# Kernel tuning notes

Hardware: AMD Instinct MI355X
Metric: run time of the kernel (lower is better)

## Reference

```python
import jax, jax.numpy as jnp
import numpy as np

N, M, H, EMB, F = 2000, 32, 64, 32, 32   # nodes, neighbors, hidden, emb_dim, node_feat_dim
T, B, HOR = 12, 4, 12                     # seq_len, batch, horizon
K = 2                                     # tcn kernel
L_SAGE = 2
DILS = (1, 2)                             # dilations for the 2 TCN blocks


def _causal_conv(x, w, b, d):
    # x: (BN, C, T), w: (C_out, C_in, K) -- causal via left padding (K-1)*d
    y = jax.lax.conv_general_dilated(
        x, w, window_strides=(1,), padding=[((K - 1) * d, 0)],
        rhs_dilation=(d,), dimension_numbers=('NCH', 'OIH', 'NCH'))
    return y + b[None, :, None]


def setup_inputs() -> dict:
    key = jax.random.key(0)
    ks = jax.random.split(key, 32)
    s = 0.05
    def g(i, shape):
        return jax.random.normal(ks[i], shape, dtype=jnp.float32) * s
    return dict(
        inputs=jax.random.normal(ks[0], (T, B, N), dtype=jnp.float32),
        node_feas=jax.random.normal(ks[1], (N, F), dtype=jnp.float32),
        node_index=jax.random.randint(ks[2], (N, M), 0, N),
        # NodeEmbeddingMLP (fc3/fc4/fc5)
        w_fc3=g(3, (F, H)), b_fc3=jnp.zeros((H,), jnp.float32),
        w_fc4=g(4, (H, H)), b_fc4=jnp.zeros((H,), jnp.float32),
        w_fc5=g(5, (H, EMB)), b_fc5=jnp.zeros((EMB,), jnp.float32),
        # node_hidden_proj
        w_nhp=g(6, (EMB, H)), b_nhp=jnp.zeros((H,), jnp.float32),
        # attention (no bias)
        w_q=g(7, (EMB, H)), w_k=g(8, (EMB, H)),
        # input_proj
        w_in=g(9, (1, H)), b_in=jnp.zeros((H,), jnp.float32),
        # GraphSAGE layers (stacked)
        sage_w_self=g(10, (L_SAGE, H, H)), sage_b_self=jnp.zeros((L_SAGE, H), jnp.float32),
        sage_w_neigh=g(11, (L_SAGE, H, H)), sage_b_neigh=jnp.zeros((L_SAGE, H), jnp.float32),
        # TCN: 2 temporal blocks, each with conv1/conv2 (OIH layout)
        tcn_w1=g(12, (2, H, H, K)), tcn_b1=jnp.zeros((2, H), jnp.float32),
        tcn_w2=g(13, (2, H, H, K)), tcn_b2=jnp.zeros((2, H), jnp.float32),
        # scalar gate + output head
        w_gate=g(14, (H, 1)), b_gate=jnp.zeros((1,), jnp.float32),
        w_out=g(15, (H, HOR)), b_out=jnp.zeros((HOR,), jnp.float32),
    )


def reference(inputs, node_feas, node_index,
              w_fc3, b_fc3, w_fc4, b_fc4, w_fc5, b_fc5,
              w_nhp, b_nhp, w_q, w_k, w_in, b_in,
              sage_w_self, sage_b_self, sage_w_neigh, sage_b_neigh,
              tcn_w1, tcn_b1, tcn_w2, tcn_b2,
              w_gate, b_gate, w_out, b_out):
    # --- node embedding MLP ---
    e = jax.nn.relu(node_feas @ w_fc3 + b_fc3)
    e = jax.nn.relu(e @ w_fc4 + b_fc4)
    e = e @ w_fc5 + b_fc5                                  # (N, EMB)

    # --- attention over sampled neighbors (learned slim adjacency) ---
    q = e @ w_q                                            # (N, H)
    k = e[node_index] @ w_k                                # (N, M, H)
    scores = jnp.einsum('nh,nmh->nm', q, k) / jnp.sqrt(jnp.float32(H))
    w_adj = jax.nn.softmax(scores, axis=1)                 # (N, M) rows sum to 1

    node_hidden = e @ w_nhp + b_nhp                        # (N, H)

    # --- reshape inputs: (T, B, N) -> (B, T, N, 1) ---
    x = jnp.transpose(inputs, (1, 0, 2)).reshape(B, T, N, 1)
    x_proj = x @ w_in + b_in                               # (B, T, N, H)
    fused = x_proj + node_hidden                           # broadcast (N, H)
    h = fused.reshape(B * T, N, H)

    # --- GraphSAGE encoder: gather neighbors, weighted aggregate ---
    for l in range(L_SAGE):
        nb = h[:, node_index]                              # (B*T, N, M, H) irregular gather
        agg = jnp.einsum('nm,bnmh->bnh', w_adj, nb)        # (B*T, N, H)
        h = jax.nn.relu(h @ sage_w_self[l] + sage_b_self[l]
                        + agg @ sage_w_neigh[l] + sage_b_neigh[l])

    mid_output = h.reshape(B, T, N, H)

    # --- TCN over time per node: (B*N, H, T) ---
    ht = jnp.transpose(mid_output, (0, 2, 3, 1)).reshape(B * N, H, T)
    for l in range(2):
        res = ht
        y = jax.nn.relu(_causal_conv(ht, tcn_w1[l], tcn_b1[l], DILS[l]))
        y = jax.nn.relu(_causal_conv(y, tcn_w2[l], tcn_b2[l], DILS[l]))
        ht = jax.nn.relu(y + res)

    h_t = ht[:, :, -1]                                     # (B*N, H) last step temporal
    h_s = mid_output[:, -1].reshape(B * N, H)              # (B*N, H) last step spatial
    gate = jax.nn.sigmoid(h_t @ w_gate + b_gate)           # (B*N, 1) scalar gate
    fused_out = gate * h_t + (1.0 - gate) * h_s

    out = fused_out @ w_out + b_out                        # (B*N, HOR)
    outputs = out.reshape(B, N, HOR).transpose(2, 0, 1).reshape(HOR, B, N)
    return outputs, mid_output, w_adj
```

## Files before the change

kernel.cpp:

```cpp
#include <hip/hip_runtime.h>
#include <math.h>


__global__ __launch_bounds__(256) void k_embed(
    const float* __restrict__ nf, const float* __restrict__ inputs,
    const float* __restrict__ w3, const float* __restrict__ b3,
    const float* __restrict__ w4, const float* __restrict__ b4,
    const float* __restrict__ w5, const float* __restrict__ b5,
    const float* __restrict__ wq, const float* __restrict__ wk,
    const float* __restrict__ wn, const float* __restrict__ bn,
    const float* __restrict__ b_in,
    const float* __restrict__ tw1, const float* __restrict__ tw2,
    const float* __restrict__ sws, const float* __restrict__ swn,
    float2* __restrict__ wtx, float4* __restrict__ wsg,
    float* __restrict__ qo, float* __restrict__ eko, float* __restrict__ nho,
    float* __restrict__ xT)
{
    const int tid = threadIdx.x;
    if (tid < 192) {
        const int id = blockIdx.x * 192 + tid;
        const int t = id / 8000, rem = id % 8000;
        const int b = rem / 2000, n2 = rem % 2000;
        xT[n2 * 48 + b * 12 + t] = inputs[id];
    }
    if (blockIdx.x < 64) {
        const int id = blockIdx.x * 256 + tid;
        const int c = id >> 12, rr = id & 4095;
        const int i = rr >> 6, o = rr & 63;
        const float* src = (c == 0) ? tw1 : (c == 1) ? tw2
                         : (c == 2) ? tw1 + 8192 : tw2 + 8192;
        wtx[id] = make_float2(src[o * 128 + i * 2], src[o * 128 + i * 2 + 1]);
    } else if (blockIdx.x < 80) {
        const int id = (blockIdx.x - 64) * 256 + tid;
        const int l = id >> 11, rr = id & 2047;
        const int k2 = rr >> 6, h = rr & 63;
        const float* S = sws + l * 4096;
        const float* Nn = swn + l * 4096;
        wsg[id] = make_float4(S[(2 * k2) * 64 + h],     Nn[(2 * k2) * 64 + h],
                              S[(2 * k2 + 1) * 64 + h], Nn[(2 * k2 + 1) * 64 + h]);
    }
    const int lane = tid & 63;
    const int n = blockIdx.x * 4 + (tid >> 6);

    float nfv = 0.f;
    if (lane < 32) nfv = nf[n * 32 + lane];

    float e1 = b3[lane];
#pragma unroll
    for (int f = 0; f < 32; ++f)
        e1 = fmaf(__shfl(nfv, f), w3[f * 64 + lane], e1);
    e1 = fmaxf(e1, 0.f);

    float e2 = b4[lane];
#pragma unroll
    for (int f = 0; f < 64; ++f)
        e2 = fmaf(__shfl(e1, f), w4[f * 64 + lane], e2);
    e2 = fmaxf(e2, 0.f);

    const int c = lane & 31;
    float ev = b5[c];
#pragma unroll
    for (int f = 0; f < 64; ++f)
        ev = fmaf(__shfl(e2, f), w5[f * 32 + c], ev);

    float qv = 0.f, ekv = 0.f, nhv = bn[lane] + b_in[lane];
#pragma unroll
    for (int f = 0; f < 32; ++f) {
        float e = __shfl(ev, f);
        qv  = fmaf(e, wq[f * 64 + lane], qv);
        ekv = fmaf(e, wk[f * 64 + lane], ekv);
        nhv = fmaf(e, wn[f * 64 + lane], nhv);
    }
    qo [n * 64 + lane] = qv;
    eko[n * 64 + lane] = ekv;
    nho[n * 64 + lane] = nhv;
}

__global__ __launch_bounds__(256) void k_front(
    const float* __restrict__ q, const float* __restrict__ ek,
    const float* __restrict__ xT, const float* __restrict__ nh2,
    const int* __restrict__ nidx,
    const float* __restrict__ sws, const float* __restrict__ sbs,
    const float* __restrict__ swn, const float* __restrict__ sbn,
    const float* __restrict__ w_in, const float4* __restrict__ wsg,
    float* __restrict__ wadj, float2* __restrict__ xa,
    float* __restrict__ base1, float* __restrict__ vecs)
{
    const int tid = threadIdx.x;
    const int lane = tid & 63, wave = tid >> 6;
    if (blockIdx.x == 500) {
        if (wave == 0) {
            const float wv = w_in[lane];
            float s1 = 0.f, n1 = 0.f;
#pragma unroll
            for (int k = 0; k < 64; ++k) {
                const float wkk = __shfl(wv, k);
                s1 = fmaf(wkk, sws[k * 64 + lane], s1);
                n1 = fmaf(wkk, swn[k * 64 + lane], n1);
            }
            vecs[lane] = s1; vecs[64 + lane] = n1;
        }
        return;
    }
    __shared__ __align__(16) float2 pair[4][64];
    const int n = blockIdx.x * 4 + wave;

    int j = 0;
    if (lane < 32) j = nidx[n * 32 + lane];
    float w;
    {
        const float4* qr = (const float4*)(q + n * 64);
        const float4* er = (const float4*)(ek + j * 64);
        float s = 0.f;
#pragma unroll
        for (int u = 0; u < 16; ++u) {
            const float4 a = qr[u], b = er[u];
            s = fmaf(a.x, b.x, s); s = fmaf(a.y, b.y, s);
            s = fmaf(a.z, b.z, s); s = fmaf(a.w, b.w, s);
        }
        s *= 0.125f;
        float mx = s;
#pragma unroll
        for (int d = 16; d >= 1; d >>= 1) mx = fmaxf(mx, __shfl_xor(mx, d));
        const float ex = expf(s - mx);
        float sum = ex;
#pragma unroll
        for (int d = 16; d >= 1; d >>= 1) sum += __shfl_xor(sum, d);
        w = ex / sum;
        if (lane < 32) wadj[n * 32 + lane] = w;
    }
    float ax = 0.f, anh = 0.f;
    const bool act = lane < 48;
#pragma unroll 8
    for (int m = 0; m < 32; ++m) {
        const int jm = __shfl(j, m);
        const float wm = __shfl(w, m);
        const float xv = act ? xT[jm * 48 + lane] : 0.f;
        ax  = fmaf(wm, xv, ax);
        anh = fmaf(wm, nh2[jm * 64 + lane], anh);
    }
    if (act) xa[n * 48 + lane] = make_float2(xT[n * 48 + lane], ax);
    pair[wave][lane] = make_float2(nh2[n * 64 + lane], anh);
    __syncthreads();

    float acc = sbs[lane] + sbn[lane];
    const float2* pw = pair[wave];
#pragma unroll
    for (int k2 = 0; k2 < 32; ++k2) {
        const float4 wv = wsg[k2 * 64 + lane];
        const float4 sv = *(const float4*)(pw + k2 * 2);
        acc = fmaf(sv.x, wv.x, acc); acc = fmaf(sv.y, wv.y, acc);
        acc = fmaf(sv.z, wv.z, acc); acc = fmaf(sv.w, wv.w, acc);
    }
    base1[n * 64 + lane] = acc;
}

__global__ __launch_bounds__(512, 8) void k_sage2(
    const float* __restrict__ base1, const float2* __restrict__ xa,
    const float* __restrict__ vecs,
    const int* __restrict__ nidx, const float* __restrict__ wadj,
    const float4* __restrict__ wsg2,
    const float* __restrict__ sbs, const float* __restrict__ sbn,
    float* __restrict__ mid)
{
    __shared__ __align__(16) float2 svp[48][64];
    const int tid = threadIdx.x, lane = tid & 63;
    const int wave = __builtin_amdgcn_readfirstlane(tid >> 6);
    const int n = blockIdx.x;
    const int bt0 = wave * 6;

    const float s1 = vecs[lane], n1 = vecs[64 + lane];
    const float bs = base1[n * 64 + lane];

    float agg[6] = {0.f, 0.f, 0.f, 0.f, 0.f, 0.f};
#pragma unroll 8
    for (int m = 0; m < 32; ++m) {
        const int j = nidx[n * 32 + m];
        const float w = wadj[n * 32 + m];
        const float bj = base1[j * 64 + lane];
        const float4* xr = (const float4*)(xa + j * 48 + bt0);
        const float4 p0 = xr[0], p1 = xr[1], p2 = xr[2];
        float t;
        t = fmaf(p0.x, s1, fmaf(p0.y, n1, bj)); agg[0] = fmaf(w, fmaxf(t, 0.f), agg[0]);
        t = fmaf(p0.z, s1, fmaf(p0.w, n1, bj)); agg[1] = fmaf(w, fmaxf(t, 0.f), agg[1]);
        t = fmaf(p1.x, s1, fmaf(p1.y, n1, bj)); agg[2] = fmaf(w, fmaxf(t, 0.f), agg[2]);
        t = fmaf(p1.z, s1, fmaf(p1.w, n1, bj)); agg[3] = fmaf(w, fmaxf(t, 0.f), agg[3]);
        t = fmaf(p2.x, s1, fmaf(p2.y, n1, bj)); agg[4] = fmaf(w, fmaxf(t, 0.f), agg[4]);
        t = fmaf(p2.z, s1, fmaf(p2.w, n1, bj)); agg[5] = fmaf(w, fmaxf(t, 0.f), agg[5]);
    }
    {
        const float4* xs = (const float4*)(xa + n * 48 + bt0);
        const float4 q0 = xs[0], q1 = xs[1], q2 = xs[2];
        svp[bt0 + 0][lane] = make_float2(fmaxf(fmaf(q0.x, s1, fmaf(q0.y, n1, bs)), 0.f), agg[0]);
        svp[bt0 + 1][lane] = make_float2(fmaxf(fmaf(q0.z, s1, fmaf(q0.w, n1, bs)), 0.f), agg[1]);
        svp[bt0 + 2][lane] = make_float2(fmaxf(fmaf(q1.x, s1, fmaf(q1.y, n1, bs)), 0.f), agg[2]);
        svp[bt0 + 3][lane] = make_float2(fmaxf(fmaf(q1.z, s1, fmaf(q1.w, n1, bs)), 0.f), agg[3]);
        svp[bt0 + 4][lane] = make_float2(fmaxf(fmaf(q2.x, s1, fmaf(q2.y, n1, bs)), 0.f), agg[4]);
        svp[bt0 + 5][lane] = make_float2(fmaxf(fmaf(q2.z, s1, fmaf(q2.w, n1, bs)), 0.f), agg[5]);
    }

    const float b2 = sbs[64 + lane] + sbn[64 + lane];
    float acc[6] = {b2, b2, b2, b2, b2, b2};
    const float4* wp = wsg2 + lane;
    const float2* s0 = svp[bt0];
#pragma unroll
    for (int k2 = 0; k2 < 32; ++k2) {
        const float4 w4 = wp[k2 * 64];
        const float4 v0 = *(const float4*)(s0 + 0 * 64 + k2 * 2);
        const float4 v1 = *(const float4*)(s0 + 1 * 64 + k2 * 2);
        const float4 v2 = *(const float4*)(s0 + 2 * 64 + k2 * 2);
        const float4 v3 = *(const float4*)(s0 + 3 * 64 + k2 * 2);
        const float4 v4 = *(const float4*)(s0 + 4 * 64 + k2 * 2);
        const float4 v5 = *(const float4*)(s0 + 5 * 64 + k2 * 2);
        acc[0] = fmaf(v0.x, w4.x, fmaf(v0.y, w4.y, fmaf(v0.z, w4.z, fmaf(v0.w, w4.w, acc[0]))));
        acc[1] = fmaf(v1.x, w4.x, fmaf(v1.y, w4.y, fmaf(v1.z, w4.z, fmaf(v1.w, w4.w, acc[1]))));
        acc[2] = fmaf(v2.x, w4.x, fmaf(v2.y, w4.y, fmaf(v2.z, w4.z, fmaf(v2.w, w4.w, acc[2]))));
        acc[3] = fmaf(v3.x, w4.x, fmaf(v3.y, w4.y, fmaf(v3.z, w4.z, fmaf(v3.w, w4.w, acc[3]))));
        acc[4] = fmaf(v4.x, w4.x, fmaf(v4.y, w4.y, fmaf(v4.z, w4.z, fmaf(v4.w, w4.w, acc[4]))));
        acc[5] = fmaf(v5.x, w4.x, fmaf(v5.y, w4.y, fmaf(v5.z, w4.z, fmaf(v5.w, w4.w, acc[5]))));
    }
#pragma unroll
    for (int r = 0; r < 6; ++r)
        mid[((bt0 + r) * 2000 + n) * 64 + lane] = fmaxf(acc[r], 0.f);
}

__global__ __launch_bounds__(256, 2) void k_tcn(
    const float* __restrict__ mid, const float2* __restrict__ wt,
    const float* __restrict__ tb1, const float* __restrict__ tb2,
    const float* __restrict__ wgate, const float* __restrict__ bgate,
    const float* __restrict__ wout, const float* __restrict__ bout,
    float* __restrict__ outp)
{
    __shared__ __align__(16) float buf[4][4][6][68];
    const int tid = threadIdx.x, lane = tid & 63;
    const int wv = __builtin_amdgcn_readfirstlane(tid >> 6);
    const int sb = blockIdx.x * 16 + wv * 4;
    const int b = sb / 2000, n0 = sb - b * 2000;
    const float* __restrict__ xb = mid + ((long)(b * 12) * 2000 + n0) * 64;

    float r[4][3];
#pragma unroll
    for (int s = 0; s < 4; ++s) {
        r[s][0] = xb[ 7 * 128000 + s * 64 + lane];
        r[s][1] = xb[ 9 * 128000 + s * 64 + lane];
        r[s][2] = xb[11 * 128000 + s * 64 + lane];
    }

    const float bs1 = tb1[lane];
    float y1[4][6];
#pragma unroll
    for (int s = 0; s < 4; ++s)
#pragma unroll
        for (int j = 0; j < 6; ++j) y1[s][j] = bs1;
#pragma unroll 2
    for (int ig = 0; ig < 16; ++ig) {
        float2 w0 = wt[(ig * 4 + 0) * 64 + lane];
        float2 w1 = wt[(ig * 4 + 1) * 64 + lane];
        float2 w2 = wt[(ig * 4 + 2) * 64 + lane];
        float2 w3 = wt[(ig * 4 + 3) * 64 + lane];
#pragma unroll
        for (int s = 0; s < 4; ++s) {
            float4 xu[7];
#pragma unroll
            for (int u = 0; u < 7; ++u)
                xu[u] = *(const float4*)(xb + (5 + u) * 128000 + s * 64 + ig * 4);
#pragma unroll
            for (int j = 0; j < 6; ++j) {
                float acc = y1[s][j];
                acc = fmaf(w0.x, xu[j].x, acc); acc = fmaf(w0.y, xu[j + 1].x, acc);
                acc = fmaf(w1.x, xu[j].y, acc); acc = fmaf(w1.y, xu[j + 1].y, acc);
                acc = fmaf(w2.x, xu[j].z, acc); acc = fmaf(w2.y, xu[j + 1].z, acc);
                acc = fmaf(w3.x, xu[j].w, acc); acc = fmaf(w3.y, xu[j + 1].w, acc);
                y1[s][j] = acc;
            }
        }
    }
#pragma unroll
    for (int s = 0; s < 4; ++s)
#pragma unroll
        for (int j = 0; j < 6; ++j)
            buf[wv][s][j][lane] = fmaxf(y1[s][j], 0.f);
    __syncthreads();

    const float bs2 = tb2[lane];
    float a[4][3];
#pragma unroll
    for (int s = 0; s < 4; ++s) { a[s][0] = bs2; a[s][1] = bs2; a[s][2] = bs2; }
#pragma unroll 2
    for (int ig = 0; ig < 16; ++ig) {
        float2 w0 = wt[4096 + (ig * 4 + 0) * 64 + lane];
        float2 w1 = wt[4096 + (ig * 4 + 1) * 64 + lane];
        float2 w2 = wt[4096 + (ig * 4 + 2) * 64 + lane];
        float2 w3 = wt[4096 + (ig * 4 + 3) * 64 + lane];
#pragma unroll
        for (int s = 0; s < 4; ++s) {
            float4 yv[6];
#pragma unroll
            for (int j = 0; j < 6; ++j)
                yv[j] = *(const float4*)&buf[wv][s][j][ig * 4];
#pragma unroll
            for (int v = 0; v < 3; ++v) {
                float acc = a[s][v];
                acc = fmaf(w0.x, yv[2*v].x, acc); acc = fmaf(w0.y, yv[2*v+1].x, acc);
                acc = fmaf(w1.x, yv[2*v].y, acc); acc = fmaf(w1.y, yv[2*v+1].y, acc);
                acc = fmaf(w2.x, yv[2*v].z, acc); acc = fmaf(w2.y, yv[2*v+1].z, acc);
                acc = fmaf(w3.x, yv[2*v].w, acc); acc = fmaf(w3.y, yv[2*v+1].w, acc);
                a[s][v] = acc;
            }
        }
    }
    float x22[4];
#pragma unroll
    for (int s = 0; s < 4; ++s) {
        const float x20 = fmaxf(fmaxf(a[s][0], 0.f) + r[s][0], 0.f);
        const float x21 = fmaxf(fmaxf(a[s][1], 0.f) + r[s][1], 0.f);
        x22[s]          = fmaxf(fmaxf(a[s][2], 0.f) + r[s][2], 0.f);
        buf[wv][s][0][lane] = x20;
        buf[wv][s][1][lane] = x21;
        buf[wv][s][2][lane] = x22[s];
    }
    __syncthreads();

    const float bs3 = tb1[64 + lane];
    float d[4][2];
#pragma unroll
    for (int s = 0; s < 4; ++s) { d[s][0] = bs3; d[s][1] = bs3; }
#pragma unroll 2
    for (int ig = 0; ig < 16; ++ig) {
        float2 w0 = wt[8192 + (ig * 4 + 0) * 64 + lane];
        float2 w1 = wt[8192 + (ig * 4 + 1) * 64 + lane];
        float2 w2 = wt[8192 + (ig * 4 + 2) * 64 + lane];
        float2 w3 = wt[8192 + (ig * 4 + 3) * 64 + lane];
#pragma unroll
        for (int s = 0; s < 4; ++s) {
            float4 x0 = *(const float4*)&buf[wv][s][0][ig * 4];
            float4 x1 = *(const float4*)&buf[wv][s][1][ig * 4];
            float4 x2 = *(const float4*)&buf[wv][s][2][ig * 4];
            float acc0 = d[s][0], acc1 = d[s][1];
            acc0 = fmaf(w0.x, x0.x, acc0); acc0 = fmaf(w0.y, x1.x, acc0);
            acc0 = fmaf(w1.x, x0.y, acc0); acc0 = fmaf(w1.y, x1.y, acc0);
            acc0 = fmaf(w2.x, x0.z, acc0); acc0 = fmaf(w2.y, x1.z, acc0);
            acc0 = fmaf(w3.x, x0.w, acc0); acc0 = fmaf(w3.y, x1.w, acc0);
            acc1 = fmaf(w0.x, x1.x, acc1); acc1 = fmaf(w0.y, x2.x, acc1);
            acc1 = fmaf(w1.x, x1.y, acc1); acc1 = fmaf(w1.y, x2.y, acc1);
            acc1 = fmaf(w2.x, x1.z, acc1); acc1 = fmaf(w2.y, x2.z, acc1);
            acc1 = fmaf(w3.x, x1.w, acc1); acc1 = fmaf(w3.y, x2.w, acc1);
            d[s][0] = acc0; d[s][1] = acc1;
        }
    }
#pragma unroll
    for (int s = 0; s < 4; ++s) {
        buf[wv][s][4][lane] = fmaxf(d[s][0], 0.f);
        buf[wv][s][5][lane] = fmaxf(d[s][1], 0.f);
    }
    __syncthreads();

    const float bs4 = tb2[64 + lane];
    float f[4] = {bs4, bs4, bs4, bs4};
#pragma unroll 2
    for (int ig = 0; ig < 16; ++ig) {
        float2 w0 = wt[12288 + (ig * 4 + 0) * 64 + lane];
        float2 w1 = wt[12288 + (ig * 4 + 1) * 64 + lane];
        float2 w2 = wt[12288 + (ig * 4 + 2) * 64 + lane];
        float2 w3 = wt[12288 + (ig * 4 + 3) * 64 + lane];
#pragma unroll
        for (int s = 0; s < 4; ++s) {
            float4 g0 = *(const float4*)&buf[wv][s][4][ig * 4];
            float4 g1 = *(const float4*)&buf[wv][s][5][ig * 4];
            float acc = f[s];
            acc = fmaf(w0.x, g0.x, acc); acc = fmaf(w0.y, g1.x, acc);
            acc = fmaf(w1.x, g0.y, acc); acc = fmaf(w1.y, g1.y, acc);
            acc = fmaf(w2.x, g0.z, acc); acc = fmaf(w2.y, g1.z, acc);
            acc = fmaf(w3.x, g0.w, acc); acc = fmaf(w3.y, g1.w, acc);
            f[s] = acc;
        }
    }

    const float wg = wgate[lane];
#pragma unroll
    for (int s = 0; s < 4; ++s) {
        const float ht = fmaxf(fmaxf(f[s], 0.f) + x22[s], 0.f);
        float p = ht * wg;
#pragma unroll
        for (int dd = 1; dd < 64; dd <<= 1) p += __shfl_xor(p, dd);
        const float g = 1.f / (1.f + expf(-(p + bgate[0])));
        buf[wv][s][5][lane] = g * ht + (1.f - g) * r[s][2];
    }
    __syncthreads();
    if (lane < 48) {
        const int s = lane / 12, h = lane - s * 12;
        float acc = bout[h];
#pragma unroll 4
        for (int ig = 0; ig < 16; ++ig) {
            const float4 f4 = *(const float4*)&buf[wv][s][5][ig * 4];
            acc = fmaf(f4.x, wout[(ig * 4 + 0) * 12 + h], acc);
            acc = fmaf(f4.y, wout[(ig * 4 + 1) * 12 + h], acc);
            acc = fmaf(f4.z, wout[(ig * 4 + 2) * 12 + h], acc);
            acc = fmaf(f4.w, wout[(ig * 4 + 3) * 12 + h], acc);
        }
        outp[h * 8000 + sb + s] = acc;
    }
}

extern "C" void kernel_launch(void* const* d_in, const int* in_sizes, int n_in,
                              void* d_out, int out_size, void* d_ws, size_t ws_size,
                              hipStream_t stream) {
    const float* inputs     = (const float*)d_in[0];
    const float* node_feas  = (const float*)d_in[1];
    const int*   node_index = (const int*)  d_in[2];
    const float* w_fc3 = (const float*)d_in[3];
    const float* b_fc3 = (const float*)d_in[4];
    const float* w_fc4 = (const float*)d_in[5];
    const float* b_fc4 = (const float*)d_in[6];
    const float* w_fc5 = (const float*)d_in[7];
    const float* b_fc5 = (const float*)d_in[8];
    const float* w_nhp = (const float*)d_in[9];
    const float* b_nhp = (const float*)d_in[10];
    const float* w_q   = (const float*)d_in[11];
    const float* w_k   = (const float*)d_in[12];
    const float* w_in  = (const float*)d_in[13];
    const float* b_in  = (const float*)d_in[14];
    const float* sws   = (const float*)d_in[15];
    const float* sbs   = (const float*)d_in[16];
    const float* swn   = (const float*)d_in[17];
    const float* sbn   = (const float*)d_in[18];
    const float* tw1   = (const float*)d_in[19];
    const float* tb1   = (const float*)d_in[20];
    const float* tw2   = (const float*)d_in[21];
    const float* tb2   = (const float*)d_in[22];
    const float* wgate = (const float*)d_in[23];
    const float* bgate = (const float*)d_in[24];
    const float* wout  = (const float*)d_in[25];
    const float* bout  = (const float*)d_in[26];

    float* out  = (float*)d_out;
    float* mid  = out + 96000;
    float* wadj = mid + 6144000;

    float*  q     = (float*)d_ws;
    float*  ek    = q     + 128000;
    float*  nh2   = ek    + 128000;
    float*  base1 = nh2   + 128000;
    float*  xT    = base1 + 128000;
    float2* xa    = (float2*)(xT + 96000);
    float*  vecs  = xT + 96000 + 192000;
    float2* wt    = (float2*)(vecs + 128);
    float4* wsg   = (float4*)(vecs + 128 + 32768);

    k_embed<<<500, 256, 0, stream>>>(node_feas, inputs, w_fc3, b_fc3, w_fc4, b_fc4,
                                     w_fc5, b_fc5, w_q, w_k, w_nhp, b_nhp, b_in,
                                     tw1, tw2, sws, swn, wt, wsg,
                                     q, ek, nh2, xT);
    k_front<<<501, 256, 0, stream>>>(q, ek, xT, nh2, node_index,
                                     sws, sbs, swn, sbn, w_in, wsg,
                                     wadj, xa, base1, vecs);
    k_sage2<<<2000, 512, 0, stream>>>(base1, xa, vecs, node_index, wadj,
                                      wsg + 2048, sbs, sbn, mid);
    k_tcn<<<500, 256, 0, stream>>>(mid, wt, tb1, tb2,
                                   wgate, bgate, wout, bout, out);
}
```

Measured before the change: 126.2 us.

## Restructure TCN kernel to stage inputs in LDS with output-channel register tiling

The TCN kernel now cooperatively loads the 7 needed time steps for 16 nodes into shared memory once, instead of each wave repeatedly reading global memory. Each thread computes 4 output channels for one node, with weights re-laid out in k_embed so that per-thread float4 weight loads are contiguous. The gate and output head are rewritten as cross-lane and cross-wave reductions through LDS. Launch bounds are raised to 4 blocks per CU. The cost is extra block-wide syncs and more register pressure.

After: 113.9 us. 9.8% less time.

```diff
diff --git a/kernel.cpp b/kernel.cpp
--- a/kernel.cpp
+++ b/kernel.cpp
@@ -12,7 +12,7 @@
     const float* __restrict__ b_in,
     const float* __restrict__ tw1, const float* __restrict__ tw2,
     const float* __restrict__ sws, const float* __restrict__ swn,
-    float2* __restrict__ wtx, float4* __restrict__ wsg,
+    float2* __restrict__ W2, float4* __restrict__ wsg,
     float* __restrict__ qo, float* __restrict__ eko, float* __restrict__ nho,
     float* __restrict__ xT)
 {
@@ -25,11 +25,12 @@
     }
     if (blockIdx.x < 64) {
         const int id = blockIdx.x * 256 + tid;
-        const int c = id >> 12, rr = id & 4095;
-        const int i = rr >> 6, o = rr & 63;
+        const int c = id >> 12, r = id & 4095;
+        const int ig = r >> 8, o = (r >> 2) & 63, ii = r & 3;
         const float* src = (c == 0) ? tw1 : (c == 1) ? tw2
                          : (c == 2) ? tw1 + 8192 : tw2 + 8192;
-        wtx[id] = make_float2(src[o * 128 + i * 2], src[o * 128 + i * 2 + 1]);
+        const int i = ig * 4 + ii;
+        W2[id] = make_float2(src[o * 128 + i * 2], src[o * 128 + i * 2 + 1]);
     } else if (blockIdx.x < 80) {
         const int id = (blockIdx.x - 64) * 256 + tid;
         const int l = id >> 11, rr = id & 2047;
@@ -198,7 +199,6 @@
         svp[bt0 + 4][lane] = make_float2(fmaxf(fmaf(q2.x, s1, fmaf(q2.y, n1, bs)), 0.f), agg[4]);
         svp[bt0 + 5][lane] = make_float2(fmaxf(fmaf(q2.z, s1, fmaf(q2.w, n1, bs)), 0.f), agg[5]);
     }
-
     const float b2 = sbs[64 + lane] + sbn[64 + lane];
     float acc[6] = {b2, b2, b2, b2, b2, b2};
     const float4* wp = wsg2 + lane;
@@ -224,181 +224,251 @@
         mid[((bt0 + r) * 2000 + n) * 64 + lane] = fmaxf(acc[r], 0.f);
 }
 
-__global__ __launch_bounds__(256, 2) void k_tcn(
-    const float* __restrict__ mid, const float2* __restrict__ wt,
+__global__ __launch_bounds__(256, 4) void k_tcn(
+    const float* __restrict__ mid, const float2* __restrict__ W2,
     const float* __restrict__ tb1, const float* __restrict__ tb2,
     const float* __restrict__ wgate, const float* __restrict__ bgate,
     const float* __restrict__ wout, const float* __restrict__ bout,
     float* __restrict__ outp)
 {
-    __shared__ __align__(16) float buf[4][4][6][68];
+    __shared__ __align__(16) float xls[9][16][68];
     const int tid = threadIdx.x, lane = tid & 63;
-    const int wv = __builtin_amdgcn_readfirstlane(tid >> 6);
-    const int sb = blockIdx.x * 16 + wv * 4;
-    const int b = sb / 2000, n0 = sb - b * 2000;
-    const float* __restrict__ xb = mid + ((long)(b * 12) * 2000 + n0) * 64;
-
-    float r[4][3];
-#pragma unroll
-    for (int s = 0; s < 4; ++s) {
-        r[s][0] = xb[ 7 * 128000 + s * 64 + lane];
-        r[s][1] = xb[ 9 * 128000 + s * 64 + lane];
-        r[s][2] = xb[11 * 128000 + s * 64 + lane];
-    }
-
-    const float bs1 = tb1[lane];
-    float y1[4][6];
-#pragma unroll
-    for (int s = 0; s < 4; ++s)
-#pragma unroll
-        for (int j = 0; j < 6; ++j) y1[s][j] = bs1;
+    const int wfl = __builtin_amdgcn_readfirstlane(tid >> 6);
+    const int h = (lane >> 4) & 3;
+    const int s = lane & 15;
+    const int bI = blockIdx.x / 125;
+    const int n0 = (blockIdx.x - bI * 125) * 16;
+    const long base = ((long)(bI * 12) * 2000 + n0) * 64;
+    const int obase = wfl * 16 + h * 4;
+    const float4* __restrict__ Wf4 = (const float4*)W2;
+
+    {
+        const int ss = tid >> 4, qq = tid & 15;
+#pragma unroll
+        for (int u = 0; u < 7; ++u) {
+            const float4 v = *(const float4*)(mid + base + (5 + u) * 128000L + ss * 64 + qq * 4);
+            *(float4*)&xls[u][ss][qq * 4] = v;
+        }
+    }
+    __syncthreads();
+
+    float y[4][6];
+    {
+        const float4 bv = *(const float4*)(tb1 + obase);
+        const float bb[4] = {bv.x, bv.y, bv.z, bv.w};
+#pragma unroll
+        for (int oo = 0; oo < 4; ++oo)
+#pragma unroll
+            for (int j = 0; j < 6; ++j) y[oo][j] = bb[oo];
 #pragma unroll 2
-    for (int ig = 0; ig < 16; ++ig) {
-        float2 w0 = wt[(ig * 4 + 0) * 64 + lane];
-        float2 w1 = wt[(ig * 4 + 1) * 64 + lane];
-        float2 w2 = wt[(ig * 4 + 2) * 64 + lane];
-        float2 w3 = wt[(ig * 4 + 3) * 64 + lane];
-#pragma unroll
-        for (int s = 0; s < 4; ++s) {
-            float4 xu[7];
+        for (int ig = 0; ig < 16; ++ig) {
+            float4 xv[7];
 #pragma unroll
             for (int u = 0; u < 7; ++u)
-                xu[u] = *(const float4*)(xb + (5 + u) * 128000 + s * 64 + ig * 4);
-#pragma unroll
-            for (int j = 0; j < 6; ++j) {
-                float acc = y1[s][j];
-                acc = fmaf(w0.x, xu[j].x, acc); acc = fmaf(w0.y, xu[j + 1].x, acc);
-                acc = fmaf(w1.x, xu[j].y, acc); acc = fmaf(w1.y, xu[j + 1].y, acc);
-                acc = fmaf(w2.x, xu[j].z, acc); acc = fmaf(w2.y, xu[j + 1].z, acc);
-                acc = fmaf(w3.x, xu[j].w, acc); acc = fmaf(w3.y, xu[j + 1].w, acc);
-                y1[s][j] = acc;
+                xv[u] = *(const float4*)&xls[u][s][ig * 4];
+#pragma unroll
+            for (int oo = 0; oo < 4; ++oo) {
+                const float4 wA = Wf4[(ig * 64 + obase + oo) * 2 + 0];
+                const float4 wB = Wf4[(ig * 64 + obase + oo) * 2 + 1];
+#pragma unroll
+                for (int j = 0; j < 6; ++j) {
+                    float acc = y[oo][j];
+                    acc = fmaf(wA.x, xv[j].x, acc); acc = fmaf(wA.y, xv[j+1].x, acc);
+                    acc = fmaf(wA.z, xv[j].y, acc); acc = fmaf(wA.w, xv[j+1].y, acc);
+                    acc = fmaf(wB.x, xv[j].z, acc); acc = fmaf(wB.y, xv[j+1].z, acc);
+                    acc = fmaf(wB.z, xv[j].w, acc); acc = fmaf(wB.w, xv[j+1].w, acc);
+                    y[oo][j] = acc;
+                }
             }
         }
     }
-#pragma unroll
-    for (int s = 0; s < 4; ++s)
-#pragma unroll
-        for (int j = 0; j < 6; ++j)
-            buf[wv][s][j][lane] = fmaxf(y1[s][j], 0.f);
-    __syncthreads();
-
-    const float bs2 = tb2[lane];
+    __syncthreads();
+    {
+        const int S1OUT[6] = {0, 1, 7, 3, 8, 5};
+#pragma unroll
+        for (int j = 0; j < 6; ++j) {
+            float4 o4;
+            o4.x = fmaxf(y[0][j], 0.f); o4.y = fmaxf(y[1][j], 0.f);
+            o4.z = fmaxf(y[2][j], 0.f); o4.w = fmaxf(y[3][j], 0.f);
+            *(float4*)&xls[S1OUT[j]][s][obase] = o4;
+        }
+    }
+    __syncthreads();
+
     float a[4][3];
-#pragma unroll
-    for (int s = 0; s < 4; ++s) { a[s][0] = bs2; a[s][1] = bs2; a[s][2] = bs2; }
+    {
+        const float4 bv = *(const float4*)(tb2 + obase);
+        const float bb[4] = {bv.x, bv.y, bv.z, bv.w};
+#pragma unroll
+        for (int oo = 0; oo < 4; ++oo)
+#pragma unroll
+            for (int v = 0; v < 3; ++v) a[oo][v] = bb[oo];
 #pragma unroll 2
-    for (int ig = 0; ig < 16; ++ig) {
-        float2 w0 = wt[4096 + (ig * 4 + 0) * 64 + lane];
-        float2 w1 = wt[4096 + (ig * 4 + 1) * 64 + lane];
-        float2 w2 = wt[4096 + (ig * 4 + 2) * 64 + lane];
-        float2 w3 = wt[4096 + (ig * 4 + 3) * 64 + lane];
-#pragma unroll
-        for (int s = 0; s < 4; ++s) {
-            float4 yv[6];
-#pragma unroll
-            for (int j = 0; j < 6; ++j)
-                yv[j] = *(const float4*)&buf[wv][s][j][ig * 4];
-#pragma unroll
-            for (int v = 0; v < 3; ++v) {
-                float acc = a[s][v];
-                acc = fmaf(w0.x, yv[2*v].x, acc); acc = fmaf(w0.y, yv[2*v+1].x, acc);
-                acc = fmaf(w1.x, yv[2*v].y, acc); acc = fmaf(w1.y, yv[2*v+1].y, acc);
-                acc = fmaf(w2.x, yv[2*v].z, acc); acc = fmaf(w2.y, yv[2*v+1].z, acc);
-                acc = fmaf(w3.x, yv[2*v].w, acc); acc = fmaf(w3.y, yv[2*v+1].w, acc);
-                a[s][v] = acc;
+        for (int ig = 0; ig < 16; ++ig) {
+            const float4 y0 = *(const float4*)&xls[0][s][ig * 4];
+            const float4 y1v = *(const float4*)&xls[1][s][ig * 4];
+            const float4 y2 = *(const float4*)&xls[7][s][ig * 4];
+            const float4 y3v = *(const float4*)&xls[3][s][ig * 4];
+            const float4 y4 = *(const float4*)&xls[8][s][ig * 4];
+            const float4 y5 = *(const float4*)&xls[5][s][ig * 4];
+#pragma unroll
+            for (int oo = 0; oo < 4; ++oo) {
+                const float4 wA = Wf4[((16 + ig) * 64 + obase + oo) * 2 + 0];
+                const float4 wB = Wf4[((16 + ig) * 64 + obase + oo) * 2 + 1];
+                float t0 = a[oo][0], t1 = a[oo][1], t2 = a[oo][2];
+                t0 = fmaf(wA.x, y0.x, t0);  t0 = fmaf(wA.y, y1v.x, t0);
+                t0 = fmaf(wA.z, y0.y, t0);  t0 = fmaf(wA.w, y1v.y, t0);
+                t0 = fmaf(wB.x, y0.z, t0);  t0 = fmaf(wB.y, y1v.z, t0);
+                t0 = fmaf(wB.z, y0.w, t0);  t0 = fmaf(wB.w, y1v.w, t0);
+                t1 = fmaf(wA.x, y2.x, t1);  t1 = fmaf(wA.y, y3v.x, t1);
+                t1 = fmaf(wA.z, y2.y, t1);  t1 = fmaf(wA.w, y3v.y, t1);
+                t1 = fmaf(wB.x, y2.z, t1);  t1 = fmaf(wB.y, y3v.z, t1);
+                t1 = fmaf(wB.z, y2.w, t1);  t1 = fmaf(wB.w, y3v.w, t1);
+                t2 = fmaf(wA.x, y4.x, t2);  t2 = fmaf(wA.y, y5.x, t2);
+                t2 = fmaf(wA.z, y4.y, t2);  t2 = fmaf(wA.w, y5.y, t2);
+                t2 = fmaf(wB.x, y4.z, t2);  t2 = fmaf(wB.y, y5.z, t2);
+                t2 = fmaf(wB.z, y4.w, t2);  t2 = fmaf(wB.w, y5.w, t2);
+                a[oo][0] = t0; a[oo][1] = t1; a[oo][2] = t2;
             }
         }
     }
-    float x22[4];
-#pragma unroll
-    for (int s = 0; s < 4; ++s) {
-        const float x20 = fmaxf(fmaxf(a[s][0], 0.f) + r[s][0], 0.f);
-        const float x21 = fmaxf(fmaxf(a[s][1], 0.f) + r[s][1], 0.f);
-        x22[s]          = fmaxf(fmaxf(a[s][2], 0.f) + r[s][2], 0.f);
-        buf[wv][s][0][lane] = x20;
-        buf[wv][s][1][lane] = x21;
-        buf[wv][s][2][lane] = x22[s];
-    }
-    __syncthreads();
-
-    const float bs3 = tb1[64 + lane];
+    __syncthreads();
+    {
+        const int RIN[3] = {2, 4, 6}, ROUT[3] = {0, 1, 7};
+#pragma unroll
+        for (int v = 0; v < 3; ++v) {
+            const float4 xr = *(const float4*)&xls[RIN[v]][s][obase];
+            float4 o4;
+            o4.x = fmaxf(fmaxf(a[0][v], 0.f) + xr.x, 0.f);
+            o4.y = fmaxf(fmaxf(a[1][v], 0.f) + xr.y, 0.f);
+            o4.z = fmaxf(fmaxf(a[2][v], 0.f) + xr.z, 0.f);
+            o4.w = fmaxf(fmaxf(a[3][v], 0.f) + xr.w, 0.f);
+            *(float4*)&xls[ROUT[v]][s][obase] = o4;
+        }
+    }
+    __syncthreads();
+
     float d[4][2];
-#pragma unroll
-    for (int s = 0; s < 4; ++s) { d[s][0] = bs3; d[s][1] = bs3; }
+    {
+        const float4 bv = *(const float4*)(tb1 + 64 + obase);
+        const float bb[4] = {bv.x, bv.y, bv.z, bv.w};
+#pragma unroll
+        for (int oo = 0; oo < 4; ++oo) { d[oo][0] = bb[oo]; d[oo][1] = bb[oo]; }
 #pragma unroll 2
-    for (int ig = 0; ig < 16; ++ig) {
-        float2 w0 = wt[8192 + (ig * 4 + 0) * 64 + lane];
-        float2 w1 = wt[8192 + (ig * 4 + 1) * 64 + lane];
-        float2 w2 = wt[8192 + (ig * 4 + 2) * 64 + lane];
-        float2 w3 = wt[8192 + (ig * 4 + 3) * 64 + lane];
-#pragma unroll
-        for (int s = 0; s < 4; ++s) {
-            float4 x0 = *(const float4*)&buf[wv][s][0][ig * 4];
-            float4 x1 = *(const float4*)&buf[wv][s][1][ig * 4];
-            float4 x2 = *(const float4*)&buf[wv][s][2][ig * 4];
-            float acc0 = d[s][0], acc1 = d[s][1];
-            acc0 = fmaf(w0.x, x0.x, acc0); acc0 = fmaf(w0.y, x1.x, acc0);
-            acc0 = fmaf(w1.x, x0.y, acc0); acc0 = fmaf(w1.y, x1.y, acc0);
-            acc0 = fmaf(w2.x, x0.z, acc0); acc0 = fmaf(w2.y, x1.z, acc0);
-            acc0 = fmaf(w3.x, x0.w, acc0); acc0 = fmaf(w3.y, x1.w, acc0);
-            acc1 = fmaf(w0.x, x1.x, acc1); acc1 = fmaf(w0.y, x2.x, acc1);
-            acc1 = fmaf(w1.x, x1.y, acc1); acc1 = fmaf(w1.y, x2.y, acc1);
-            acc1 = fmaf(w2.x, x1.z, acc1); acc1 = fmaf(w2.y, x2.z, acc1);
-            acc1 = fmaf(w3.x, x1.w, acc1); acc1 = fmaf(w3.y, x2.w, acc1);
-            d[s][0] = acc0; d[s][1] = acc1;
-        }
-    }
-#pragma unroll
-    for (int s = 0; s < 4; ++s) {
-        buf[wv][s][4][lane] = fmaxf(d[s][0], 0.f);
-        buf[wv][s][5][lane] = fmaxf(d[s][1], 0.f);
-    }
-    __syncthreads();
-
-    const float bs4 = tb2[64 + lane];
-    float f[4] = {bs4, bs4, bs4, bs4};
+        for (int ig = 0; ig < 16; ++ig) {
+            const float4 x0 = *(const float4*)&xls[0][s][ig * 4];
+            const float4 x1 = *(const float4*)&xls[1][s][ig * 4];
+            const float4 x2 = *(const float4*)&xls[7][s][ig * 4];
+#pragma unroll
+            for (int oo = 0; oo < 4; ++oo) {
+                const float4 wA = Wf4[((32 + ig) * 64 + obase + oo) * 2 + 0];
+                const float4 wB = Wf4[((32 + ig) * 64 + obase + oo) * 2 + 1];
+                float t0 = d[oo][0], t1 = d[oo][1];
+                t0 = fmaf(wA.x, x0.x, t0);  t0 = fmaf(wA.y, x1.x, t0);
+                t0 = fmaf(wA.z, x0.y, t0);  t0 = fmaf(wA.w, x1.y, t0);
+                t0 = fmaf(wB.x, x0.z, t0);  t0 = fmaf(wB.y, x1.z, t0);
+                t0 = fmaf(wB.z, x0.w, t0);  t0 = fmaf(wB.w, x1.w, t0);
+                t1 = fmaf(wA.x, x1.x, t1);  t1 = fmaf(wA.y, x2.x, t1);
+                t1 = fmaf(wA.z, x1.y, t1);  t1 = fmaf(wA.w, x2.y, t1);
+                t1 = fmaf(wB.x, x1.z, t1);  t1 = fmaf(wB.y, x2.z, t1);
+                t1 = fmaf(wB.z, x1.w, t1);  t1 = fmaf(wB.w, x2.w, t1);
+                d[oo][0] = t0; d[oo][1] = t1;
+            }
+        }
+    }
+    {
+        float4 o4;
+        o4.x = fmaxf(d[0][0], 0.f); o4.y = fmaxf(d[1][0], 0.f);
+        o4.z = fmaxf(d[2][0], 0.f); o4.w = fmaxf(d[3][0], 0.f);
+        *(float4*)&xls[3][s][obase] = o4;
+        o4.x = fmaxf(d[0][1], 0.f); o4.y = fmaxf(d[1][1], 0.f);
+        o4.z = fmaxf(d[2][1], 0.f); o4.w = fmaxf(d[3][1], 0.f);
+        *(float4*)&xls[8][s][obase] = o4;
+    }
+    __syncthreads();
+
+    float f[4];
+    {
+        const float4 bv = *(const float4*)(tb2 + 64 + obase);
+        f[0] = bv.x; f[1] = bv.y; f[2] = bv.z; f[3] = bv.w;
 #pragma unroll 2
-    for (int ig = 0; ig < 16; ++ig) {
-        float2 w0 = wt[12288 + (ig * 4 + 0) * 64 + lane];
-        float2 w1 = wt[12288 + (ig * 4 + 1) * 64 + lane];
-        float2 w2 = wt[12288 + (ig * 4 + 2) * 64 + lane];
-        float2 w3 = wt[12288 + (ig * 4 + 3) * 64 + lane];
-#pragma unroll
-        for (int s = 0; s < 4; ++s) {
-            float4 g0 = *(const float4*)&buf[wv][s][4][ig * 4];
-            float4 g1 = *(const float4*)&buf[wv][s][5][ig * 4];
-            float acc = f[s];
-            acc = fmaf(w0.x, g0.x, acc); acc = fmaf(w0.y, g1.x, acc);
-            acc = fmaf(w1.x, g0.y, acc); acc = fmaf(w1.y, g1.y, acc);
-            acc = fmaf(w2.x, g0.z, acc); acc = fmaf(w2.y, g1.z, acc);
-            acc = fmaf(w3.x, g0.w, acc); acc = fmaf(w3.y, g1.w, acc);
-            f[s] = acc;
-        }
-    }
-
-    const float wg = wgate[lane];
-#pragma unroll
-    for (int s = 0; s < 4; ++s) {
-        const float ht = fmaxf(fmaxf(f[s], 0.f) + x22[s], 0.f);
-        float p = ht * wg;
-#pragma unroll
-        for (int dd = 1; dd < 64; dd <<= 1) p += __shfl_xor(p, dd);
-        const float g = 1.f / (1.f + expf(-(p + bgate[0])));
-        buf[wv][s][5][lane] = g * ht + (1.f - g) * r[s][2];
-    }
-    __syncthreads();
-    if (lane < 48) {
-        const int s = lane / 12, h = lane - s * 12;
-        float acc = bout[h];
-#pragma unroll 4
         for (int ig = 0; ig < 16; ++ig) {
-            const float4 f4 = *(const float4*)&buf[wv][s][5][ig * 4];
-            acc = fmaf(f4.x, wout[(ig * 4 + 0) * 12 + h], acc);
-            acc = fmaf(f4.y, wout[(ig * 4 + 1) * 12 + h], acc);
-            acc = fmaf(f4.z, wout[(ig * 4 + 2) * 12 + h], acc);
-            acc = fmaf(f4.w, wout[(ig * 4 + 3) * 12 + h], acc);
-        }
-        outp[h * 8000 + sb + s] = acc;
+            const float4 g0 = *(const float4*)&xls[3][s][ig * 4];
+            const float4 g1 = *(const float4*)&xls[8][s][ig * 4];
+#pragma unroll
+            for (int oo = 0; oo < 4; ++oo) {
+                const float4 wA = Wf4[((48 + ig) * 64 + obase + oo) * 2 + 0];
+                const float4 wB = Wf4[((48 + ig) * 64 + obase + oo) * 2 + 1];
+                float t0 = f[oo];
+                t0 = fmaf(wA.x, g0.x, t0);  t0 = fmaf(wA.y, g1.x, t0);
+                t0 = fmaf(wA.z, g0.y, t0);  t0 = fmaf(wA.w, g1.y, t0);
+                t0 = fmaf(wB.x, g0.z, t0);  t0 = fmaf(wB.y, g1.z, t0);
+                t0 = fmaf(wB.z, g0.w, t0);  t0 = fmaf(wB.w, g1.w, t0);
+                f[oo] = t0;
+            }
+        }
+    }
+    float ht[4];
+    {
+        const float4 xr = *(const float4*)&xls[7][s][obase];
+        ht[0] = fmaxf(fmaxf(f[0], 0.f) + xr.x, 0.f);
+        ht[1] = fmaxf(fmaxf(f[1], 0.f) + xr.y, 0.f);
+        ht[2] = fmaxf(fmaxf(f[2], 0.f) + xr.z, 0.f);
+        ht[3] = fmaxf(fmaxf(f[3], 0.f) + xr.w, 0.f);
+    }
+
+    float* pbuf = &xls[2][0][0];
+    {
+        const float4 wg4 = *(const float4*)(wgate + obase);
+        float p = ht[0] * wg4.x + ht[1] * wg4.y + ht[2] * wg4.z + ht[3] * wg4.w;
+        p += __shfl_xor(p, 16); p += __shfl_xor(p, 32);
+        if (h == 0) pbuf[wfl * 16 + s] = p;
+    }
+    __syncthreads();
+    const float ptot = pbuf[s] + pbuf[16 + s] + pbuf[32 + s] + pbuf[48 + s];
+    const float g = 1.f / (1.f + expf(-(ptot + bgate[0])));
+    float fo[4];
+    {
+        const float4 hs = *(const float4*)&xls[6][s][obase];
+        fo[0] = g * ht[0] + (1.f - g) * hs.x;
+        fo[1] = g * ht[1] + (1.f - g) * hs.y;
+        fo[2] = g * ht[2] + (1.f - g) * hs.z;
+        fo[3] = g * ht[3] + (1.f - g) * hs.w;
+    }
+    float po[12];
+#pragma unroll
+    for (int h2 = 0; h2 < 12; ++h2) po[h2] = 0.f;
+#pragma unroll
+    for (int oo = 0; oo < 4; ++oo) {
+        const float* wr = wout + (obase + oo) * 12;
+        const float4 w0 = *(const float4*)(wr);
+        const float4 w1 = *(const float4*)(wr + 4);
+        const float4 w2 = *(const float4*)(wr + 8);
+        po[0] = fmaf(fo[oo], w0.x, po[0]);  po[1] = fmaf(fo[oo], w0.y, po[1]);
+        po[2] = fmaf(fo[oo], w0.z, po[2]);  po[3] = fmaf(fo[oo], w0.w, po[3]);
+        po[4] = fmaf(fo[oo], w1.x, po[4]);  po[5] = fmaf(fo[oo], w1.y, po[5]);
+        po[6] = fmaf(fo[oo], w1.z, po[6]);  po[7] = fmaf(fo[oo], w1.w, po[7]);
+        po[8] = fmaf(fo[oo], w2.x, po[8]);  po[9] = fmaf(fo[oo], w2.y, po[9]);
+        po[10] = fmaf(fo[oo], w2.z, po[10]); po[11] = fmaf(fo[oo], w2.w, po[11]);
+    }
+#pragma unroll
+    for (int h2 = 0; h2 < 12; ++h2) {
+        po[h2] += __shfl_xor(po[h2], 16);
+        po[h2] += __shfl_xor(po[h2], 32);
+    }
+    float* pobuf = &xls[4][0][0];
+    if (h == 0) {
+#pragma unroll
+        for (int h2 = 0; h2 < 12; ++h2)
+            pobuf[(wfl * 12 + h2) * 16 + s] = po[h2];
+    }
+    __syncthreads();
+    if (tid < 192) {
+        const int h2 = tid >> 4, sq = tid & 15;
+        const float r = pobuf[(0 * 12 + h2) * 16 + sq] + pobuf[(1 * 12 + h2) * 16 + sq]
+                      + pobuf[(2 * 12 + h2) * 16 + sq] + pobuf[(3 * 12 + h2) * 16 + sq]
+                      + bout[h2];
+        outp[h2 * 8000 + bI * 2000 + n0 + sq] = r;
     }
 }
 
@@ -444,18 +514,18 @@
     float*  xT    = base1 + 128000;
     float2* xa    = (float2*)(xT + 96000);
     float*  vecs  = xT + 96000 + 192000;
-    float2* wt    = (float2*)(vecs + 128);
+    float2* W2    = (float2*)(vecs + 128);
     float4* wsg   = (float4*)(vecs + 128 + 32768);
 
     k_embed<<<500, 256, 0, stream>>>(node_feas, inputs, w_fc3, b_fc3, w_fc4, b_fc4,
                                      w_fc5, b_fc5, w_q, w_k, w_nhp, b_nhp, b_in,
-                                     tw1, tw2, sws, swn, wt, wsg,
+                                     tw1, tw2, sws, swn, W2, wsg,
                                      q, ek, nh2, xT);
     k_front<<<501, 256, 0, stream>>>(q, ek, xT, nh2, node_index,
                                      sws, sbs, swn, sbn, w_in, wsg,
                                      wadj, xa, base1, vecs);
     k_sage2<<<2000, 512, 0, stream>>>(base1, xa, vecs, node_index, wadj,
                                       wsg + 2048, sbs, sbn, mid);
-    k_tcn<<<500, 256, 0, stream>>>(mid, wt, tb1, tb2,
+    k_tcn<<<500, 256, 0, stream>>>(mid, W2, tb1, tb2,
                                    wgate, bgate, wout, bout, out);
 }
```
